# Optimization experiments

Measured on AMD Instinct MI355X. Metric: run time of the kernel, lower is better.

## Reference

```python
import jax, jax.numpy as jnp
import numpy as np

DIM = 128
NUM_LAYERS = 2
FF_MULT = 4
RADIUS = 0.2
K = 8
B, N, L = 8, 2048, 4096
NEG = -1e30


def setup_inputs() -> dict:
    key = jax.random.key(0)
    ks = jax.random.split(key, 12)
    C = DIM
    s = 1.0 / np.sqrt(C)
    w = lambda k, shape, sc: jax.random.normal(k, shape, dtype=jnp.float32) * sc
    inp = {
        "q_xyz": jax.random.uniform(ks[0], (B, N, 3), dtype=jnp.float32),
        "q_feat": jax.random.normal(ks[1], (B, N, C), dtype=jnp.float32),
        "kv_xyz": jax.random.uniform(ks[2], (B, L, 3), dtype=jnp.float32),
        "kv_feat": jax.random.normal(ks[3], (B, L, C), dtype=jnp.float32),
        "kv_pad": jnp.zeros((B, L), dtype=bool),
        # PointTransformerConv params (stacked over layers)
        "W_lin": w(ks[4], (NUM_LAYERS, C, C), s),   # value projection (with bias)
        "b_lin": jnp.zeros((NUM_LAYERS, C), jnp.float32),
        "W_src": w(ks[5], (NUM_LAYERS, C, C), s),   # lin_src, no bias
        "W_dst": w(ks[6], (NUM_LAYERS, C, C), s),   # lin_dst, no bias
        "W_attn": w(ks[7], (NUM_LAYERS, C, C), s),  # attn_nn = Linear+ReLU
        "b_attn": jnp.zeros((NUM_LAYERS, C), jnp.float32),
        "ln1_g": jnp.ones((NUM_LAYERS, C), jnp.float32),
        "ln1_b": jnp.zeros((NUM_LAYERS, C), jnp.float32),
        "W_ff1": w(ks[8], (NUM_LAYERS, C, FF_MULT * C), s),
        "b_ff1": jnp.zeros((NUM_LAYERS, FF_MULT * C), jnp.float32),
        "W_ff2": w(ks[9], (NUM_LAYERS, FF_MULT * C, C), 1.0 / np.sqrt(FF_MULT * C)),
        "b_ff2": jnp.zeros((NUM_LAYERS, C), jnp.float32),
        "ln2_g": jnp.ones((NUM_LAYERS, C), jnp.float32),
        "ln2_b": jnp.zeros((NUM_LAYERS, C), jnp.float32),
    }
    return inp


def _layernorm(x, g, b):
    mu = x.mean(-1, keepdims=True)
    var = ((x - mu) ** 2).mean(-1, keepdims=True)
    return (x - mu) * jax.lax.rsqrt(var + 1e-5) * g + b


def _gather(feats, idx):
    # feats: [B, L, C], idx: [B, N, K] -> [B, N, K, C]
    b, n, k = idx.shape
    g = jnp.take_along_axis(feats, idx.reshape(b, n * k)[:, :, None], axis=1)
    return g.reshape(b, n, k, feats.shape[-1])


def _forward(q_xyz, q_feat, kv_xyz, kv_feat, kv_pad,
             W_lin, b_lin, W_src, W_dst, W_attn, b_attn,
             ln1_g, ln1_b, W_ff1, b_ff1, W_ff2, b_ff2, ln2_g, ln2_b):
    # radius neighbor search (per-batch, fixed K neighbors with validity mask)
    d2 = jnp.sum((q_xyz[:, :, None, :] - kv_xyz[:, None, :, :]) ** 2, axis=-1)  # [B,N,L]
    valid_pair = (d2 <= RADIUS * RADIUS) & (~kv_pad)[:, None, :]
    negd = jnp.where(valid_pair, -d2, NEG)
    negv, idx = jax.lax.top_k(negd, K)          # [B,N,K] nearest-in-ball
    evalid = negv > 0.5 * NEG                   # edge validity mask [B,N,K]

    out = q_feat
    for i in range(NUM_LAYERS):
        # PointTransformerConv, pos_nn = ZeroPos => delta = 0
        aj = _gather(kv_feat @ W_src[i], idx)                    # [B,N,K,C]
        vj = _gather(kv_feat @ W_lin[i] + b_lin[i], idx)         # [B,N,K,C]
        ai = out @ W_dst[i]                                      # [B,N,C]
        logits = jax.nn.relu((ai[:, :, None, :] - aj) @ W_attn[i] + b_attn[i])
        logits = jnp.where(evalid[..., None], logits, NEG)
        m = logits.max(axis=2, keepdims=True)
        e = jnp.exp(logits - m) * evalid[..., None]
        attn = e / jnp.maximum(e.sum(axis=2, keepdims=True), 1e-9)  # per-channel softmax over neighbors
        upd = jnp.sum(attn * vj, axis=2)                         # [B,N,C] scatter-add over edges
        out = _layernorm(out + upd, ln1_g[i], ln1_b[i])
        h = jax.nn.gelu(out @ W_ff1[i] + b_ff1[i], approximate=False)
        out = _layernorm(out + h @ W_ff2[i] + b_ff2[i], ln2_g[i], ln2_b[i])
    return out


def reference(q_xyz, q_feat, kv_xyz, kv_feat, kv_pad,
              W_lin, b_lin, W_src, W_dst, W_attn, b_attn,
              ln1_g, ln1_b, W_ff1, b_ff1, W_ff2, b_ff2, ln2_g, ln2_b):
    return _forward(q_xyz, q_feat, kv_xyz, kv_feat, kv_pad,
                    W_lin, b_lin, W_src, W_dst, W_attn, b_attn,
                    ln1_g, ln1_b, W_ff1, b_ff1, W_ff2, b_ff2, ln2_g, ln2_b)
```

## Files before the change

### kernel.cpp

```cpp
#include <hip/hip_runtime.h>
#include <hip/hip_bf16.h>
#include <math.h>

#define DIM 128
#define BB 8
#define NN 2048
#define LL 4096
#define KK 8

typedef __hip_bfloat16 bf16;
typedef unsigned long long ull;
typedef __attribute__((ext_vector_type(8))) short short8;
typedef __attribute__((ext_vector_type(4))) float float4v;

__device__ __forceinline__ float toF(float x){ return x; }
__device__ __forceinline__ float toF(bf16 x){ return __bfloat162float(x); }
__device__ __forceinline__ void st(float* p, float v){ *p = v; }
__device__ __forceinline__ void st(bf16*  p, float v){ *p = __float2bfloat16(v); }
__device__ __forceinline__ unsigned short f2bf(float f){
  union { bf16 b; unsigned short u; } cv; cv.b = __float2bfloat16(f); return cv.u;
}

__device__ __forceinline__ float gelu_exact(float x){
  return 0.5f * x * (1.0f + erff(x * 0.70710678118654752f));
}

__device__ __forceinline__ float waveSum64(float v){
  #pragma unroll
  for (int o = 32; o > 0; o >>= 1) v += __shfl_xor(v, o, 64);
  return v;
}
__device__ __forceinline__ float quadSum16(float v){
  #pragma unroll
  for (int o = 8; o > 0; o >>= 1) v += __shfl_xor(v, o, 64);
  return v;
}

__device__ __forceinline__ void topk_insert_u(ull (&m)[KK], ull key){
  m[KK-1] = key;
  #pragma unroll
  for (int t = KK-1; t > 0; --t){
    if (m[t] < m[t-1]){ ull tmp = m[t]; m[t] = m[t-1]; m[t-1] = tmp; }
  }
}

#define NCELL 5
#define NC3 125
__global__ __launch_bounds__(1024) void knn_bin(const float* __restrict__ kv_xyz,
                                                float4* __restrict__ bpts,
                                                int* __restrict__ offs )
{
  __shared__ int cnt[NC3];
  __shared__ int off[NC3+1];
  const int b = blockIdx.x;
  const int tid = threadIdx.x;
  if (tid < NC3) cnt[tid] = 0;
  __syncthreads();
  const float* kvp = kv_xyz + (size_t)b * LL * 3;
  float px[4], py[4], pz[4]; int pc[4];
  #pragma unroll
  for (int i = 0; i < 4; i++){
    const int e = tid + i*1024;
    px[i] = kvp[3*e]; py[i] = kvp[3*e+1]; pz[i] = kvp[3*e+2];
    const int cx = min((int)(px[i]*5.f), 4);
    const int cy = min((int)(py[i]*5.f), 4);
    const int cz = min((int)(pz[i]*5.f), 4);
    pc[i] = (cz*5 + cy)*5 + cx;
    atomicAdd(&cnt[pc[i]], 1);
  }
  __syncthreads();
  if (tid == 0){
    int acc = 0;
    for (int c = 0; c < NC3; c++){ off[c] = acc; acc += cnt[c]; }
    off[NC3] = acc;
  }
  __syncthreads();
  if (tid < NC3) cnt[tid] = 0;
  __syncthreads();
  float4* dst = bpts + (size_t)b * LL;
  #pragma unroll
  for (int i = 0; i < 4; i++){
    const int e = tid + i*1024;
    const int pos = off[pc[i]] + atomicAdd(&cnt[pc[i]], 1);
    dst[pos] = make_float4(px[i], py[i], pz[i], __int_as_float(e));
  }
  if (tid < NC3 + 1) offs[b*126 + tid] = off[tid];
}

#define QBLK 8
#define SPL 32
__global__ __launch_bounds__(256) void knn_query(const float* __restrict__ q_xyz,
                                                 const float4* __restrict__ bpts,
                                                 const int* __restrict__ offs,
                                                 int* __restrict__ idx)
{
  __shared__ ull cd[QBLK*257];
  const int tid  = threadIdx.x;
  const int s    = tid >> 3;
  const int qloc = tid & 7;
  const int b    = blockIdx.y;
  const int qbase = blockIdx.x * QBLK;
  const size_t qo = ((size_t)b * NN + qbase + qloc) * 3;
  const float qx = q_xyz[qo], qy = q_xyz[qo+1], qz = q_xyz[qo+2];
  const ull THRKEY = ((ull)0x3D23D70Bu << 32);
  ull kthr = THRKEY;
  ull m[KK];
  #pragma unroll
  for (int k = 0; k < KK; k++) m[k] = ~0ULL;
  const int qcx = min((int)(qx*5.f), 4);
  const int qcy = min((int)(qy*5.f), 4);
  const int qcz = min((int)(qz*5.f), 4);
  const int* ofb = offs + b*126;
  const float4* bp = bpts + (size_t)b * LL;
  const int cx0 = max(qcx-1, 0), cx1 = min(qcx+1, 4);
  for (int cz = max(qcz-1,0); cz <= min(qcz+1,4); cz++){
    for (int cy = max(qcy-1,0); cy <= min(qcy+1,4); cy++){
      const int rowc = (cz*5 + cy)*5;
      const int pstart = ofb[rowc + cx0];
      const int pend   = ofb[rowc + cx1 + 1];
      for (int p = pstart + s; p < pend; p += SPL){
        const float4 pt = bp[p];
        const float dx = qx - pt.x, dy = qy - pt.y, dz = qz - pt.z;
        const float d2 = dx*dx + dy*dy + dz*dz;
        const ull key = ((ull)__float_as_uint(d2) << 32) | (unsigned)__float_as_int(pt.w);
        if (key < kthr){
          topk_insert_u(m, key);
          kthr = (m[KK-1] < THRKEY) ? m[KK-1] : THRKEY;
        }
      }
    }
  }
  #pragma unroll
  for (int k = 0; k < KK; k++) cd[qloc*257 + s*8 + k] = m[k];
  __syncthreads();
  if (tid < 64){
    const int q = tid >> 3, g = tid & 7;
    ull mm[KK];
    #pragma unroll
    for (int k = 0; k < KK; k++) mm[k] = ~0ULL;
    #pragma unroll
    for (int u = 0; u < 4; u++){
      const int sl = g + 8*u;
      #pragma unroll
      for (int k = 0; k < KK; k++){
        const ull key = cd[q*257 + sl*8 + k];
        if (key < mm[KK-1]) topk_insert_u(mm, key);
      }
    }
    #pragma unroll
    for (int k = 0; k < KK; k++) cd[q*257 + g*8 + k] = mm[k];
    if (tid < QBLK){
      ull f[KK];
      #pragma unroll
      for (int k = 0; k < KK; k++) f[k] = ~0ULL;
      for (int j = 0; j < 64; j++){
        const ull key = cd[tid*257 + j];
        if (key < f[KK-1]) topk_insert_u(f, key);
      }
      const int q = b * NN + qbase + tid;
      #pragma unroll
      for (int k = 0; k < KK; k++) idx[q*KK + k] = (int)(unsigned)(f[k] & 0xFFFFFFFFu);
    }
  }
}

__device__ __forceinline__ void packOne(const float* __restrict__ src,
                                        bf16* __restrict__ dst, int idx, int nshift){
  const int k = idx >> nshift;
  const int n = idx & ((1 << nshift) - 1);
  const int N = 1 << nshift;
  st(&dst[((size_t)(k>>3)*N + n)*8 + (k&7)], src[idx]);
}

__global__ __launch_bounds__(256) void prep_weights(const float* __restrict__ Wlin,
                                                    const float* __restrict__ Wff1,
                                                    const float* __restrict__ Wff2,
                                                    const float* __restrict__ Wsrc,
                                                    const float* __restrict__ Wdst,
                                                    const float* __restrict__ Wattn,
                                                    bf16* __restrict__ WlinP,
                                                    bf16* __restrict__ Wff1P,
                                                    bf16* __restrict__ Wff2P,
                                                    bf16* __restrict__ WsaP,
                                                    bf16* __restrict__ WdaP)
{
  __shared__ float row[2][DIM];
  const int bid = blockIdx.x;
  if (bid < 1152){
    int i = bid*256 + threadIdx.x;
    if (i < 32768){
      const int l = i >> 14, r = i & 16383;
      packOne(Wlin + (size_t)l*16384, WlinP + (size_t)l*16384, r, 7);
    } else if (i < 163840){
      i -= 32768;
      const int l = i >> 16, r = i & 65535;
      packOne(Wff1 + (size_t)l*65536, Wff1P + (size_t)l*65536, r, 9);
    } else if (i < 294912){
      i -= 163840;
      const int l = i >> 16, r = i & 65535;
      packOne(Wff2 + (size_t)l*65536, Wff2P + (size_t)l*65536, r, 7);
    }
  } else {
    const int half = threadIdx.x >> 7;
    const int c = threadIdx.x & 127;
    const int tt = (bid - 1152)*2 + half;
    const int r = tt & 127, which = (tt >> 7) & 1, lay = tt >> 8;
    const float* Wx = (which ? Wdst : Wsrc) + (size_t)lay*DIM*DIM;
    const float* Wa = Wattn + (size_t)lay*DIM*DIM;
    row[half][c] = Wx[r*DIM + c];
    __syncthreads();
    float acc = 0.f;
    for (int j = 0; j < DIM; j++) acc = fmaf(row[half][j], Wa[j*DIM + c], acc);
    bf16* dst = (which ? WdaP : WsaP) + (size_t)lay*DIM*DIM;
    st(&dst[((size_t)(r>>3)*DIM + c)*8 + (r&7)], acc);
  }
}

__device__ __forceinline__ void stage_A_f32(const float* __restrict__ A, size_t r0,
                                            int kd, int kc, unsigned short* As, int tid){
  #pragma unroll
  for (int i = 0; i < 8; i++){
    const int f = tid + i*256;
    const int row = f >> 5, c4 = (f & 31) * 4;
    const float4 v = *(const float4*)&A[(r0+row)*kd + kc + c4];
    uint2 u;
    u.x = (unsigned)f2bf(v.x) | ((unsigned)f2bf(v.y) << 16);
    u.y = (unsigned)f2bf(v.z) | ((unsigned)f2bf(v.w) << 16);
    *(uint2*)&As[row*136 + c4] = u;
  }
}
__device__ __forceinline__ void stage_A_bf16(const bf16* __restrict__ A, size_t r0,
                                             int kd, int kc, unsigned short* As, int tid){
  #pragma unroll
  for (int i = 0; i < 8; i++){
    const int f = tid + i*256;
    const int row = f >> 5, c4 = (f & 31) * 4;
    *(uint2*)&As[row*136 + c4] = *(const uint2*)&A[(r0+row)*kd + kc + c4];
  }
}

template<typename TA, int NDIM, bool GELU>
__global__ __launch_bounds__(256) void mfma_single(const TA* __restrict__ A,
                                                   const bf16* __restrict__ Wp,
                                                   const float* __restrict__ bias,
                                                   bf16* __restrict__ Y)
{
  __shared__ __align__(16) unsigned short As[64*136];
  const int tid = threadIdx.x;
  const size_t r0 = (size_t)blockIdx.x * 64;
  const int nblk = blockIdx.y * 128;
  if (sizeof(TA) == 4) stage_A_f32((const float*)A, r0, 128, 0, As, tid);
  else                 stage_A_bf16((const bf16*)A, r0, 128, 0, As, tid);
  __syncthreads();
  const int wid = tid >> 6, ln = tid & 63, qd = ln >> 4, cl = ln & 15;
  float4v acc[8];
  #pragma unroll
  for (int t = 0; t < 8; t++) acc[t] = (float4v){0.f,0.f,0.f,0.f};
  #pragma unroll
  for (int ks = 0; ks < 4; ks++){
    const short8 a = *(const short8*)&As[(wid*16 + cl)*136 + (ks*4 + qd)*8];
    const short8* wb = (const short8*)Wp + (size_t)(ks*4 + qd)*NDIM + nblk + cl;
    #pragma unroll
    for (int t = 0; t < 8; t++){
      const short8 b = wb[t*16];
      acc[t] = __builtin_amdgcn_mfma_f32_16x16x32_bf16(a, b, acc[t], 0, 0, 0);
    }
  }
  #pragma unroll
  for (int t = 0; t < 8; t++){
    const int col = nblk + t*16 + cl;
    const float bv = bias ? bias[col] : 0.f;
    #pragma unroll
    for (int r = 0; r < 4; r++){
      const size_t row = r0 + wid*16 + qd*4 + r;
      float v = acc[t][r] + bv;
      if (GELU) v = gelu_exact(v);
      st(&Y[row*NDIM + col], v);
    }
  }
}

__global__ __launch_bounds__(256) void mfma_dual_qa(const float* __restrict__ kvf,
                                                    const float* __restrict__ featIn,
                                                    const bf16* __restrict__ Wp0,
                                                    const bf16* __restrict__ Wp1,
                                                    const bf16* __restrict__ WpQ,
                                                    const float* __restrict__ bias1,
                                                    bf16* __restrict__ Y0,
                                                    bf16* __restrict__ Y1,
                                                    bf16* __restrict__ Yq)
{
  __shared__ __align__(16) unsigned short As[64*136];
  const int tid = threadIdx.x;
  const int wid = tid >> 6, ln = tid & 63, qd = ln >> 4, cl = ln & 15;
  if (blockIdx.x < 512){
    const size_t r0 = (size_t)blockIdx.x * 64;
    stage_A_f32(kvf, r0, 128, 0, As, tid);
    __syncthreads();
    float4v ac0[8], ac1[8];
    #pragma unroll
    for (int t = 0; t < 8; t++){ ac0[t] = (float4v){0.f,0.f,0.f,0.f}; ac1[t] = (float4v){0.f,0.f,0.f,0.f}; }
    #pragma unroll
    for (int ks = 0; ks < 4; ks++){
      const short8 a = *(const short8*)&As[(wid*16 + cl)*136 + (ks*4 + qd)*8];
      const size_t wo = (size_t)(ks*4 + qd)*DIM + cl;
      const short8* wb0 = (const short8*)Wp0 + wo;
      const short8* wb1 = (const short8*)Wp1 + wo;
      #pragma unroll
      for (int t = 0; t < 8; t++){
        const short8 b0 = wb0[t*16];
        ac0[t] = __builtin_amdgcn_mfma_f32_16x16x32_bf16(a, b0, ac0[t], 0, 0, 0);
        const short8 b1 = wb1[t*16];
        ac1[t] = __builtin_amdgcn_mfma_f32_16x16x32_bf16(a, b1, ac1[t], 0, 0, 0);
      }
    }
    #pragma unroll
    for (int t = 0; t < 8; t++){
      const int col = t*16 + cl;
      const float bv = bias1[col];
      #pragma unroll
      for (int r = 0; r < 4; r++){
        const size_t row = r0 + wid*16 + qd*4 + r;
        st(&Y0[row*DIM + col], ac0[t][r]);
        st(&Y1[row*DIM + col], ac1[t][r] + bv);
      }
    }
  } else {
    const size_t r0 = (size_t)(blockIdx.x - 512) * 64;
    stage_A_f32(featIn, r0, 128, 0, As, tid);
    __syncthreads();
    float4v acc[8];
    #pragma unroll
    for (int t = 0; t < 8; t++) acc[t] = (float4v){0.f,0.f,0.f,0.f};
    #pragma unroll
    for (int ks = 0; ks < 4; ks++){
      const short8 a = *(const short8*)&As[(wid*16 + cl)*136 + (ks*4 + qd)*8];
      const short8* wb = (const short8*)WpQ + (size_t)(ks*4 + qd)*DIM + cl;
      #pragma unroll
      for (int t = 0; t < 8; t++){
        const short8 b = wb[t*16];
        acc[t] = __builtin_amdgcn_mfma_f32_16x16x32_bf16(a, b, acc[t], 0, 0, 0);
      }
    }
    #pragma unroll
    for (int t = 0; t < 8; t++){
      const int col = t*16 + cl;
      #pragma unroll
      for (int r = 0; r < 4; r++){
        const size_t row = r0 + wid*16 + qd*4 + r;
        st(&Yq[row*DIM + col], acc[t][r]);
      }
    }
  }
}

__global__ __launch_bounds__(256) void mfma_ff2ln(const bf16* __restrict__ A,
                                                  const bf16* __restrict__ Wp,
                                                  const float* __restrict__ b2,
                                                  const bf16* __restrict__ resid,
                                                  const float* __restrict__ g,
                                                  const float* __restrict__ bb,
                                                  float* __restrict__ Y)
{
  __shared__ __align__(16) unsigned short As[64*136];
  const int tid = threadIdx.x;
  const size_t r0 = (size_t)blockIdx.x * 64;
  const int wid = tid >> 6, ln = tid & 63, qd = ln >> 4, cl = ln & 15;
  float4v acc[8];
  #pragma unroll
  for (int t = 0; t < 8; t++) acc[t] = (float4v){0.f,0.f,0.f,0.f};
  for (int kc = 0; kc < 512; kc += 128){
    __syncthreads();
    stage_A_bf16(A, r0, 512, kc, As, tid);
    __syncthreads();
    const int k8c = kc >> 3;
    #pragma unroll
    for (int ks = 0; ks < 4; ks++){
      const short8 a = *(const short8*)&As[(wid*16 + cl)*136 + (ks*4 + qd)*8];
      const short8* wb = (const short8*)Wp + (size_t)(k8c + ks*4 + qd)*DIM + cl;
      #pragma unroll
      for (int t = 0; t < 8; t++){
        const short8 b = wb[t*16];
        acc[t] = __builtin_amdgcn_mfma_f32_16x16x32_bf16(a, b, acc[t], 0, 0, 0);
      }
    }
  }
  float v[8][4];
  #pragma unroll
  for (int t = 0; t < 8; t++){
    const int col = t*16 + cl;
    const float bv = b2[col];
    #pragma unroll
    for (int r = 0; r < 4; r++){
      const size_t row = r0 + wid*16 + qd*4 + r;
      v[t][r] = acc[t][r] + bv + toF(resid[row*DIM + col]);
    }
  }
  #pragma unroll
  for (int r = 0; r < 4; r++){
    float s = 0.f;
    #pragma unroll
    for (int t = 0; t < 8; t++) s += v[t][r];
    const float mu = quadSum16(s) * (1.f/DIM);
    float q = 0.f;
    #pragma unroll
    for (int t = 0; t < 8; t++){ const float d = v[t][r] - mu; q += d*d; }
    const float inv = rsqrtf(quadSum16(q) * (1.f/DIM) + 1e-5f);
    const size_t row = r0 + wid*16 + qd*4 + r;
    #pragma unroll
    for (int t = 0; t < 8; t++){
      const int col = t*16 + cl;
      Y[row*DIM + col] = (v[t][r] - mu) * inv * g[col] + bb[col];
    }
  }
}

__global__ __launch_bounds__(256) void attn_ln1(const bf16* __restrict__ qA,
                                                const bf16* __restrict__ srcA,
                                                const bf16* __restrict__ linp,
                                                const int* __restrict__ idx,
                                                const float* __restrict__ b_attn,
                                                const float* __restrict__ feat,
                                                const float* __restrict__ g,
                                                const float* __restrict__ bb,
                                                bf16* __restrict__ out1)
{
  const int tid = threadIdx.x;
  const int wv = tid >> 6, ln = tid & 63;
  const int q = blockIdx.x * 4 + wv;
  const int b = q >> 11;
  const bf16* sbase = srcA + (size_t)b * LL * DIM;
  const bf16* vbase = linp + (size_t)b * LL * DIM;
  const int c0 = ln, c1 = ln + 64;
  const float qa0 = toF(qA[(size_t)q*DIM + c0]) + b_attn[c0];
  const float qa1 = toF(qA[(size_t)q*DIM + c1]) + b_attn[c1];
  int ids[KK]; float l0[KK], l1[KK];
  float m0 = -1e30f, m1 = -1e30f;
  #pragma unroll
  for (int k = 0; k < KK; k++){
    const int id = idx[q*KK + k]; ids[k] = id;
    if (id >= 0){
      const float s0 = toF(sbase[(size_t)id*DIM + c0]);
      const float s1 = toF(sbase[(size_t)id*DIM + c1]);
      l0[k] = fmaxf(qa0 - s0, 0.f); m0 = fmaxf(m0, l0[k]);
      l1[k] = fmaxf(qa1 - s1, 0.f); m1 = fmaxf(m1, l1[k]);
    } else { l0[k] = 0.f; l1[k] = 0.f; }
  }
  float sum0 = 0.f, sum1 = 0.f, upd0 = 0.f, upd1 = 0.f;
  #pragma unroll
  for (int k = 0; k < KK; k++) if (ids[k] >= 0){
    const float e0 = expf(l0[k] - m0); l0[k] = e0; sum0 += e0;
    const float e1 = expf(l1[k] - m1); l1[k] = e1; sum1 += e1;
  }
  if (sum0 > 0.f){
    const float i0 = 1.f / sum0, i1 = 1.f / sum1;
    #pragma unroll
    for (int k = 0; k < KK; k++) if (ids[k] >= 0){
      upd0 = fmaf(l0[k]*i0, toF(vbase[(size_t)ids[k]*DIM + c0]), upd0);
      upd1 = fmaf(l1[k]*i1, toF(vbase[(size_t)ids[k]*DIM + c1]), upd1);
    }
  }
  const float x0 = feat[(size_t)q*DIM + c0] + upd0;
  const float x1 = feat[(size_t)q*DIM + c1] + upd1;
  const float mu = waveSum64(x0 + x1) * (1.f/DIM);
  const float d0 = x0 - mu, d1 = x1 - mu;
  const float var = waveSum64(d0*d0 + d1*d1) * (1.f/DIM);
  const float inv = rsqrtf(var + 1e-5f);
  st(&out1[(size_t)q*DIM + c0], d0 * inv * g[c0] + bb[c0]);
  st(&out1[(size_t)q*DIM + c1], d1 * inv * g[c1] + bb[c1]);
}

extern "C" void kernel_launch(void* const* d_in, const int* in_sizes, int n_in,
                              void* d_out, int out_size, void* d_ws, size_t ws_size,
                              hipStream_t stream)
{
  const float* q_xyz  = (const float*)d_in[0];
  const float* q_feat = (const float*)d_in[1];
  const float* kv_xyz = (const float*)d_in[2];
  const float* kv_feat= (const float*)d_in[3];
  const float* W_lin  = (const float*)d_in[5];
  const float* b_lin  = (const float*)d_in[6];
  const float* W_src  = (const float*)d_in[7];
  const float* W_dst  = (const float*)d_in[8];
  const float* W_attn = (const float*)d_in[9];
  const float* b_attn = (const float*)d_in[10];
  const float* ln1_g  = (const float*)d_in[11];
  const float* ln1_b  = (const float*)d_in[12];
  const float* W_ff1  = (const float*)d_in[13];
  const float* b_ff1  = (const float*)d_in[14];
  const float* W_ff2  = (const float*)d_in[15];
  const float* b_ff2  = (const float*)d_in[16];
  const float* ln2_g  = (const float*)d_in[17];
  const float* ln2_b  = (const float*)d_in[18];
  float* out = (float*)d_out;

  const int MQ  = BB * NN;
  const int MKV = BB * LL;

  char* p = (char*)d_ws;
  int*    idxb  = (int*)p;    p += (size_t)MQ * KK * 4;
  float4* bpts  = (float4*)p; p += (size_t)BB * LL * 16;
  int*    boffs = (int*)p;    p += (size_t)BB * 126 * 4;
  bf16*  WsaP  = (bf16*)p;  p += (size_t)2 * DIM * DIM * 2;
  bf16*  WdaP  = (bf16*)p;  p += (size_t)2 * DIM * DIM * 2;
  bf16*  WlinP = (bf16*)p;  p += (size_t)2 * DIM * DIM * 2;
  bf16*  Wff1P = (bf16*)p;  p += (size_t)2 * DIM * 4*DIM * 2;
  bf16*  Wff2P = (bf16*)p;  p += (size_t)2 * 4*DIM * DIM * 2;
  float* feat  = (float*)p; p += (size_t)MQ * DIM * 4;
  bf16*  out1  = (bf16*)p;  p += (size_t)MQ * DIM * 2;
  bf16*  srcA  = (bf16*)p;  p += (size_t)MKV * DIM * 2;
  bf16*  linp  = (bf16*)p;  p += (size_t)MKV * DIM * 2;
  bf16*  qA    = (bf16*)p;  p += (size_t)MQ * DIM * 2;
  bf16*  hbuf  = srcA;

  knn_bin<<<BB, 1024, 0, stream>>>(kv_xyz, bpts, boffs);
  knn_query<<<dim3(NN/QBLK, BB), 256, 0, stream>>>(q_xyz, bpts, boffs, idxb);
  prep_weights<<<1152 + 256, 256, 0, stream>>>(W_lin, W_ff1, W_ff2, W_src, W_dst,
                                               W_attn, WlinP, Wff1P, Wff2P, WsaP, WdaP);

  for (int i = 0; i < 2; i++){
    const size_t w128 = (size_t)i * DIM * DIM;
    const size_t w512 = (size_t)i * DIM * 4*DIM;
    const float* featIn = (i == 0) ? q_feat : feat;

    mfma_dual_qa<<<MKV/64 + MQ/64, 256, 0, stream>>>(kv_feat, featIn,
        WsaP + w128, WlinP + w128, WdaP + w128, b_lin + i*DIM, srcA, linp, qA);
    attn_ln1<<<MQ/4, 256, 0, stream>>>(qA, srcA, linp, idxb, b_attn + i*DIM, featIn,
                                       ln1_g + i*DIM, ln1_b + i*DIM, out1);
    mfma_single<bf16, 512, true><<<dim3(MQ/64, 4), 256, 0, stream>>>(
        out1, Wff1P + w512, b_ff1 + i*4*DIM, hbuf);
    float* ydst = (i == 1) ? out : feat;
    mfma_ff2ln<<<MQ/64, 256, 0, stream>>>(hbuf, Wff2P + w512, b_ff2 + i*DIM, out1,
                                          ln2_g + i*DIM, ln2_b + i*DIM, ydst);
  }
}
```

Before: 302.6 us.

## Fuse attention, LN1, FFN and LN2 into one kernel; sort queries by grid cell

Attention aggregation, the first layernorm, the FF1+GELU GEMM and the FF2+layernorm GEMM now run in one per-wave kernel. Each wave keeps its 16 rows and the 512-wide hidden activations in LDS, so the out1 and hidden buffers no longer make global-memory round trips and two launches per layer go away. Separately, query points are binned by spatial cell so each knn_query block works on nearby queries, which should make neighbour scans more uniform within a block and cache-friendlier. The trade-off is much more LDS per block (about 87 KB), which lowers occupancy, and 16 serial attention rows per wave before the MFMA work starts.

```diff
diff --git a/kernel.cpp b/kernel.cpp
--- a/kernel.cpp
+++ b/kernel.cpp
@@ -15,6 +15,9 @@
 
 __device__ __forceinline__ float toF(float x){ return x; }
 __device__ __forceinline__ float toF(bf16 x){ return __bfloat162float(x); }
+__device__ __forceinline__ float bfuToF(unsigned short u){
+  return __uint_as_float((unsigned)u << 16);
+}
 __device__ __forceinline__ void st(float* p, float v){ *p = v; }
 __device__ __forceinline__ void st(bf16*  p, float v){ *p = __float2bfloat16(v); }
 __device__ __forceinline__ unsigned short f2bf(float f){
@@ -44,47 +47,80 @@
   }
 }
 
-#define NCELL 5
 #define NC3 125
 __global__ __launch_bounds__(1024) void knn_bin(const float* __restrict__ kv_xyz,
+                                                const float* __restrict__ q_xyz,
                                                 float4* __restrict__ bpts,
-                                                int* __restrict__ offs )
+                                                int* __restrict__ offs ,
+                                                int* __restrict__ qsrt )
 {
   __shared__ int cnt[NC3];
   __shared__ int off[NC3+1];
-  const int b = blockIdx.x;
+  const int b   = blockIdx.x & 7;
+  const int role= blockIdx.x >> 3;
   const int tid = threadIdx.x;
   if (tid < NC3) cnt[tid] = 0;
   __syncthreads();
-  const float* kvp = kv_xyz + (size_t)b * LL * 3;
-  float px[4], py[4], pz[4]; int pc[4];
-  #pragma unroll
-  for (int i = 0; i < 4; i++){
-    const int e = tid + i*1024;
-    px[i] = kvp[3*e]; py[i] = kvp[3*e+1]; pz[i] = kvp[3*e+2];
-    const int cx = min((int)(px[i]*5.f), 4);
-    const int cy = min((int)(py[i]*5.f), 4);
-    const int cz = min((int)(pz[i]*5.f), 4);
-    pc[i] = (cz*5 + cy)*5 + cx;
-    atomicAdd(&cnt[pc[i]], 1);
-  }
-  __syncthreads();
-  if (tid == 0){
-    int acc = 0;
-    for (int c = 0; c < NC3; c++){ off[c] = acc; acc += cnt[c]; }
-    off[NC3] = acc;
-  }
-  __syncthreads();
-  if (tid < NC3) cnt[tid] = 0;
-  __syncthreads();
-  float4* dst = bpts + (size_t)b * LL;
-  #pragma unroll
-  for (int i = 0; i < 4; i++){
-    const int e = tid + i*1024;
-    const int pos = off[pc[i]] + atomicAdd(&cnt[pc[i]], 1);
-    dst[pos] = make_float4(px[i], py[i], pz[i], __int_as_float(e));
-  }
-  if (tid < NC3 + 1) offs[b*126 + tid] = off[tid];
+  if (role == 0){
+    const float* kvp = kv_xyz + (size_t)b * LL * 3;
+    float px[4], py[4], pz[4]; int pc[4];
+    #pragma unroll
+    for (int i = 0; i < 4; i++){
+      const int e = tid + i*1024;
+      px[i] = kvp[3*e]; py[i] = kvp[3*e+1]; pz[i] = kvp[3*e+2];
+      const int cx = min((int)(px[i]*5.f), 4);
+      const int cy = min((int)(py[i]*5.f), 4);
+      const int cz = min((int)(pz[i]*5.f), 4);
+      pc[i] = (cz*5 + cy)*5 + cx;
+      atomicAdd(&cnt[pc[i]], 1);
+    }
+    __syncthreads();
+    if (tid == 0){
+      int acc = 0;
+      for (int c = 0; c < NC3; c++){ off[c] = acc; acc += cnt[c]; }
+      off[NC3] = acc;
+    }
+    __syncthreads();
+    if (tid < NC3) cnt[tid] = 0;
+    __syncthreads();
+    float4* dst = bpts + (size_t)b * LL;
+    #pragma unroll
+    for (int i = 0; i < 4; i++){
+      const int e = tid + i*1024;
+      const int pos = off[pc[i]] + atomicAdd(&cnt[pc[i]], 1);
+      dst[pos] = make_float4(px[i], py[i], pz[i], __int_as_float(e));
+    }
+    if (tid < NC3 + 1) offs[b*126 + tid] = off[tid];
+  } else {
+    const float* qp = q_xyz + (size_t)b * NN * 3;
+    int pc[2];
+    #pragma unroll
+    for (int i = 0; i < 2; i++){
+      const int e = tid + i*1024;
+      const float x = qp[3*e], y = qp[3*e+1], z = qp[3*e+2];
+      const int cx = min((int)(x*5.f), 4);
+      const int cy = min((int)(y*5.f), 4);
+      const int cz = min((int)(z*5.f), 4);
+      pc[i] = (cz*5 + cy)*5 + cx;
+      atomicAdd(&cnt[pc[i]], 1);
+    }
+    __syncthreads();
+    if (tid == 0){
+      int acc = 0;
+      for (int c = 0; c < NC3; c++){ off[c] = acc; acc += cnt[c]; }
+      off[NC3] = acc;
+    }
+    __syncthreads();
+    if (tid < NC3) cnt[tid] = 0;
+    __syncthreads();
+    int* dst = qsrt + (size_t)b * NN;
+    #pragma unroll
+    for (int i = 0; i < 2; i++){
+      const int e = tid + i*1024;
+      const int pos = off[pc[i]] + atomicAdd(&cnt[pc[i]], 1);
+      dst[pos] = e;
+    }
+  }
 }
 
 #define QBLK 8
@@ -92,6 +128,7 @@
 __global__ __launch_bounds__(256) void knn_query(const float* __restrict__ q_xyz,
                                                  const float4* __restrict__ bpts,
                                                  const int* __restrict__ offs,
+                                                 const int* __restrict__ qsrt,
                                                  int* __restrict__ idx)
 {
   __shared__ ull cd[QBLK*257];
@@ -100,7 +137,8 @@
   const int qloc = tid & 7;
   const int b    = blockIdx.y;
   const int qbase = blockIdx.x * QBLK;
-  const size_t qo = ((size_t)b * NN + qbase + qloc) * 3;
+  const int qid = qsrt[b*NN + qbase + qloc];
+  const size_t qo = ((size_t)b * NN + qid) * 3;
   const float qx = q_xyz[qo], qy = q_xyz[qo+1], qz = q_xyz[qo+2];
   const ull THRKEY = ((ull)0x3D23D70Bu << 32);
   ull kthr = THRKEY;
@@ -157,9 +195,9 @@
         const ull key = cd[tid*257 + j];
         if (key < f[KK-1]) topk_insert_u(f, key);
       }
-      const int q = b * NN + qbase + tid;
-      #pragma unroll
-      for (int k = 0; k < KK; k++) idx[q*KK + k] = (int)(unsigned)(f[k] & 0xFFFFFFFFu);
+      const int oq = b * NN + qsrt[b*NN + qbase + tid];
+      #pragma unroll
+      for (int k = 0; k < KK; k++) idx[oq*KK + k] = (int)(unsigned)(f[k] & 0xFFFFFFFFu);
     }
   }
 }
@@ -229,56 +267,6 @@
     *(uint2*)&As[row*136 + c4] = u;
   }
 }
-__device__ __forceinline__ void stage_A_bf16(const bf16* __restrict__ A, size_t r0,
-                                             int kd, int kc, unsigned short* As, int tid){
-  #pragma unroll
-  for (int i = 0; i < 8; i++){
-    const int f = tid + i*256;
-    const int row = f >> 5, c4 = (f & 31) * 4;
-    *(uint2*)&As[row*136 + c4] = *(const uint2*)&A[(r0+row)*kd + kc + c4];
-  }
-}
-
-template<typename TA, int NDIM, bool GELU>
-__global__ __launch_bounds__(256) void mfma_single(const TA* __restrict__ A,
-                                                   const bf16* __restrict__ Wp,
-                                                   const float* __restrict__ bias,
-                                                   bf16* __restrict__ Y)
-{
-  __shared__ __align__(16) unsigned short As[64*136];
-  const int tid = threadIdx.x;
-  const size_t r0 = (size_t)blockIdx.x * 64;
-  const int nblk = blockIdx.y * 128;
-  if (sizeof(TA) == 4) stage_A_f32((const float*)A, r0, 128, 0, As, tid);
-  else                 stage_A_bf16((const bf16*)A, r0, 128, 0, As, tid);
-  __syncthreads();
-  const int wid = tid >> 6, ln = tid & 63, qd = ln >> 4, cl = ln & 15;
-  float4v acc[8];
-  #pragma unroll
-  for (int t = 0; t < 8; t++) acc[t] = (float4v){0.f,0.f,0.f,0.f};
-  #pragma unroll
-  for (int ks = 0; ks < 4; ks++){
-    const short8 a = *(const short8*)&As[(wid*16 + cl)*136 + (ks*4 + qd)*8];
-    const short8* wb = (const short8*)Wp + (size_t)(ks*4 + qd)*NDIM + nblk + cl;
-    #pragma unroll
-    for (int t = 0; t < 8; t++){
-      const short8 b = wb[t*16];
-      acc[t] = __builtin_amdgcn_mfma_f32_16x16x32_bf16(a, b, acc[t], 0, 0, 0);
-    }
-  }
-  #pragma unroll
-  for (int t = 0; t < 8; t++){
-    const int col = nblk + t*16 + cl;
-    const float bv = bias ? bias[col] : 0.f;
-    #pragma unroll
-    for (int r = 0; r < 4; r++){
-      const size_t row = r0 + wid*16 + qd*4 + r;
-      float v = acc[t][r] + bv;
-      if (GELU) v = gelu_exact(v);
-      st(&Y[row*NDIM + col], v);
-    }
-  }
-}
 
 __global__ __launch_bounds__(256) void mfma_dual_qa(const float* __restrict__ kvf,
                                                     const float* __restrict__ featIn,
@@ -354,34 +342,108 @@
   }
 }
 
-__global__ __launch_bounds__(256) void mfma_ff2ln(const bf16* __restrict__ A,
-                                                  const bf16* __restrict__ Wp,
-                                                  const float* __restrict__ b2,
-                                                  const bf16* __restrict__ resid,
-                                                  const float* __restrict__ g,
-                                                  const float* __restrict__ bb,
-                                                  float* __restrict__ Y)
+__global__ __launch_bounds__(256) void attn_ff(const bf16* __restrict__ qA,
+                                               const bf16* __restrict__ srcA,
+                                               const bf16* __restrict__ linp,
+                                               const int* __restrict__ idx,
+                                               const float* __restrict__ b_attn,
+                                               const float* __restrict__ featIn,
+                                               const float* __restrict__ g1,
+                                               const float* __restrict__ bb1,
+                                               const bf16* __restrict__ W1p,
+                                               const float* __restrict__ b1,
+                                               const bf16* __restrict__ W2p,
+                                               const float* __restrict__ b2,
+                                               const float* __restrict__ g2,
+                                               const float* __restrict__ bb2,
+                                               float* __restrict__ Y)
 {
-  __shared__ __align__(16) unsigned short As[64*136];
+  __shared__ __align__(16) unsigned short As[4][16*136];
+  __shared__ __align__(16) unsigned short Hs[4][4][16*136];
   const int tid = threadIdx.x;
-  const size_t r0 = (size_t)blockIdx.x * 64;
-  const int wid = tid >> 6, ln = tid & 63, qd = ln >> 4, cl = ln & 15;
-  float4v acc[8];
-  #pragma unroll
-  for (int t = 0; t < 8; t++) acc[t] = (float4v){0.f,0.f,0.f,0.f};
-  for (int kc = 0; kc < 512; kc += 128){
-    __syncthreads();
-    stage_A_bf16(A, r0, 512, kc, As, tid);
-    __syncthreads();
-    const int k8c = kc >> 3;
+  const int w = tid >> 6, ln = tid & 63, qd = ln >> 4, cl = ln & 15;
+  const int q0 = blockIdx.x * 64 + w * 16;
+  for (int j = 0; j < 16; j++){
+    const int q = q0 + j;
+    const int b = q >> 11;
+    const bf16* sbase = srcA + (size_t)b * LL * DIM;
+    const bf16* vbase = linp + (size_t)b * LL * DIM;
+    const int c0 = ln, c1 = ln + 64;
+    const float qa0 = toF(qA[(size_t)q*DIM + c0]) + b_attn[c0];
+    const float qa1 = toF(qA[(size_t)q*DIM + c1]) + b_attn[c1];
+    int ids[KK]; float l0[KK], l1[KK];
+    float m0 = -1e30f, m1 = -1e30f;
+    #pragma unroll
+    for (int k = 0; k < KK; k++){
+      const int id = idx[q*KK + k]; ids[k] = id;
+      if (id >= 0){
+        l0[k] = fmaxf(qa0 - toF(sbase[(size_t)id*DIM + c0]), 0.f); m0 = fmaxf(m0, l0[k]);
+        l1[k] = fmaxf(qa1 - toF(sbase[(size_t)id*DIM + c1]), 0.f); m1 = fmaxf(m1, l1[k]);
+      } else { l0[k] = 0.f; l1[k] = 0.f; }
+    }
+    float sum0 = 0.f, sum1 = 0.f, upd0 = 0.f, upd1 = 0.f;
+    #pragma unroll
+    for (int k = 0; k < KK; k++) if (ids[k] >= 0){
+      const float e0 = expf(l0[k] - m0); l0[k] = e0; sum0 += e0;
+      const float e1 = expf(l1[k] - m1); l1[k] = e1; sum1 += e1;
+    }
+    if (sum0 > 0.f){
+      const float i0 = 1.f / sum0, i1 = 1.f / sum1;
+      #pragma unroll
+      for (int k = 0; k < KK; k++) if (ids[k] >= 0){
+        upd0 = fmaf(l0[k]*i0, toF(vbase[(size_t)ids[k]*DIM + c0]), upd0);
+        upd1 = fmaf(l1[k]*i1, toF(vbase[(size_t)ids[k]*DIM + c1]), upd1);
+      }
+    }
+    const float x0 = featIn[(size_t)q*DIM + c0] + upd0;
+    const float x1 = featIn[(size_t)q*DIM + c1] + upd1;
+    const float mu = waveSum64(x0 + x1) * (1.f/DIM);
+    const float d0 = x0 - mu, d1 = x1 - mu;
+    const float var = waveSum64(d0*d0 + d1*d1) * (1.f/DIM);
+    const float inv = rsqrtf(var + 1e-5f);
+    As[w][j*136 + c0] = f2bf(d0 * inv * g1[c0] + bb1[c0]);
+    As[w][j*136 + c1] = f2bf(d1 * inv * g1[c1] + bb1[c1]);
+  }
+  #pragma unroll
+  for (int half = 0; half < 2; half++){
+    float4v acc[16];
+    #pragma unroll
+    for (int t = 0; t < 16; t++) acc[t] = (float4v){0.f,0.f,0.f,0.f};
     #pragma unroll
     for (int ks = 0; ks < 4; ks++){
-      const short8 a = *(const short8*)&As[(wid*16 + cl)*136 + (ks*4 + qd)*8];
-      const short8* wb = (const short8*)Wp + (size_t)(k8c + ks*4 + qd)*DIM + cl;
+      const short8 a = *(const short8*)&As[w][cl*136 + (ks*4 + qd)*8];
+      const short8* wb = (const short8*)W1p + (size_t)(ks*4 + qd)*512 + half*256 + cl;
+      #pragma unroll
+      for (int t = 0; t < 16; t++){
+        const short8 b = wb[t*16];
+        acc[t] = __builtin_amdgcn_mfma_f32_16x16x32_bf16(a, b, acc[t], 0, 0, 0);
+      }
+    }
+    #pragma unroll
+    for (int t = 0; t < 16; t++){
+      const int col = half*256 + t*16 + cl;
+      const float bv = b1[col];
+      const int chunk = half*2 + (t >> 3);
+      #pragma unroll
+      for (int r = 0; r < 4; r++){
+        Hs[w][chunk][(qd*4 + r)*136 + (t & 7)*16 + cl] = f2bf(gelu_exact(acc[t][r] + bv));
+      }
+    }
+  }
+  float4v a2[8];
+  #pragma unroll
+  for (int t = 0; t < 8; t++) a2[t] = (float4v){0.f,0.f,0.f,0.f};
+  #pragma unroll
+  for (int chunk = 0; chunk < 4; chunk++){
+    #pragma unroll
+    for (int ks = 0; ks < 4; ks++){
+      const short8 a = *(const short8*)&Hs[w][chunk][cl*136 + (ks*4 + qd)*8];
+      const int k8 = chunk*16 + ks*4 + qd;
+      const short8* wb = (const short8*)W2p + (size_t)k8*DIM + cl;
       #pragma unroll
       for (int t = 0; t < 8; t++){
         const short8 b = wb[t*16];
-        acc[t] = __builtin_amdgcn_mfma_f32_16x16x32_bf16(a, b, acc[t], 0, 0, 0);
+        a2[t] = __builtin_amdgcn_mfma_f32_16x16x32_bf16(a, b, a2[t], 0, 0, 0);
       }
     }
   }
@@ -392,8 +454,7 @@
     const float bv = b2[col];
     #pragma unroll
     for (int r = 0; r < 4; r++){
-      const size_t row = r0 + wid*16 + qd*4 + r;
-      v[t][r] = acc[t][r] + bv + toF(resid[row*DIM + col]);
+      v[t][r] = a2[t][r] + bv + bfuToF(As[w][(qd*4 + r)*136 + col]);
     }
   }
   #pragma unroll
@@ -402,72 +463,17 @@
     #pragma unroll
     for (int t = 0; t < 8; t++) s += v[t][r];
     const float mu = quadSum16(s) * (1.f/DIM);
-    float q = 0.f;
-    #pragma unroll
-    for (int t = 0; t < 8; t++){ const float d = v[t][r] - mu; q += d*d; }
-    const float inv = rsqrtf(quadSum16(q) * (1.f/DIM) + 1e-5f);
-    const size_t row = r0 + wid*16 + qd*4 + r;
+    float qv = 0.f;
+    #pragma unroll
+    for (int t = 0; t < 8; t++){ const float d = v[t][r] - mu; qv += d*d; }
+    const float inv = rsqrtf(quadSum16(qv) * (1.f/DIM) + 1e-5f);
+    const size_t row = q0 + qd*4 + r;
     #pragma unroll
     for (int t = 0; t < 8; t++){
       const int col = t*16 + cl;
-      Y[row*DIM + col] = (v[t][r] - mu) * inv * g[col] + bb[col];
-    }
-  }
-}
-
-__global__ __launch_bounds__(256) void attn_ln1(const bf16* __restrict__ qA,
-                                                const bf16* __restrict__ srcA,
-                                                const bf16* __restrict__ linp,
-                                                const int* __restrict__ idx,
-                                                const float* __restrict__ b_attn,
-                                                const float* __restrict__ feat,
-                                                const float* __restrict__ g,
-                                                const float* __restrict__ bb,
-                                                bf16* __restrict__ out1)
-{
-  const int tid = threadIdx.x;
-  const int wv = tid >> 6, ln = tid & 63;
-  const int q = blockIdx.x * 4 + wv;
-  const int b = q >> 11;
-  const bf16* sbase = srcA + (size_t)b * LL * DIM;
-  const bf16* vbase = linp + (size_t)b * LL * DIM;
-  const int c0 = ln, c1 = ln + 64;
-  const float qa0 = toF(qA[(size_t)q*DIM + c0]) + b_attn[c0];
-  const float qa1 = toF(qA[(size_t)q*DIM + c1]) + b_attn[c1];
-  int ids[KK]; float l0[KK], l1[KK];
-  float m0 = -1e30f, m1 = -1e30f;
-  #pragma unroll
-  for (int k = 0; k < KK; k++){
-    const int id = idx[q*KK + k]; ids[k] = id;
-    if (id >= 0){
-      const float s0 = toF(sbase[(size_t)id*DIM + c0]);
-      const float s1 = toF(sbase[(size_t)id*DIM + c1]);
-      l0[k] = fmaxf(qa0 - s0, 0.f); m0 = fmaxf(m0, l0[k]);
-      l1[k] = fmaxf(qa1 - s1, 0.f); m1 = fmaxf(m1, l1[k]);
-    } else { l0[k] = 0.f; l1[k] = 0.f; }
-  }
-  float sum0 = 0.f, sum1 = 0.f, upd0 = 0.f, upd1 = 0.f;
-  #pragma unroll
-  for (int k = 0; k < KK; k++) if (ids[k] >= 0){
-    const float e0 = expf(l0[k] - m0); l0[k] = e0; sum0 += e0;
-    const float e1 = expf(l1[k] - m1); l1[k] = e1; sum1 += e1;
-  }
-  if (sum0 > 0.f){
-    const float i0 = 1.f / sum0, i1 = 1.f / sum1;
-    #pragma unroll
-    for (int k = 0; k < KK; k++) if (ids[k] >= 0){
-      upd0 = fmaf(l0[k]*i0, toF(vbase[(size_t)ids[k]*DIM + c0]), upd0);
-      upd1 = fmaf(l1[k]*i1, toF(vbase[(size_t)ids[k]*DIM + c1]), upd1);
-    }
-  }
-  const float x0 = feat[(size_t)q*DIM + c0] + upd0;
-  const float x1 = feat[(size_t)q*DIM + c1] + upd1;
-  const float mu = waveSum64(x0 + x1) * (1.f/DIM);
-  const float d0 = x0 - mu, d1 = x1 - mu;
-  const float var = waveSum64(d0*d0 + d1*d1) * (1.f/DIM);
-  const float inv = rsqrtf(var + 1e-5f);
-  st(&out1[(size_t)q*DIM + c0], d0 * inv * g[c0] + bb[c0]);
-  st(&out1[(size_t)q*DIM + c1], d1 * inv * g[c1] + bb[c1]);
+      Y[row*DIM + col] = (v[t][r] - mu) * inv * g2[col] + bb2[col];
+    }
+  }
 }
 
 extern "C" void kernel_launch(void* const* d_in, const int* in_sizes, int n_in,
@@ -501,20 +507,19 @@
   int*    idxb  = (int*)p;    p += (size_t)MQ * KK * 4;
   float4* bpts  = (float4*)p; p += (size_t)BB * LL * 16;
   int*    boffs = (int*)p;    p += (size_t)BB * 126 * 4;
+  int*    qsrt  = (int*)p;    p += (size_t)BB * NN * 4;
   bf16*  WsaP  = (bf16*)p;  p += (size_t)2 * DIM * DIM * 2;
   bf16*  WdaP  = (bf16*)p;  p += (size_t)2 * DIM * DIM * 2;
   bf16*  WlinP = (bf16*)p;  p += (size_t)2 * DIM * DIM * 2;
   bf16*  Wff1P = (bf16*)p;  p += (size_t)2 * DIM * 4*DIM * 2;
   bf16*  Wff2P = (bf16*)p;  p += (size_t)2 * 4*DIM * DIM * 2;
   float* feat  = (float*)p; p += (size_t)MQ * DIM * 4;
-  bf16*  out1  = (bf16*)p;  p += (size_t)MQ * DIM * 2;
   bf16*  srcA  = (bf16*)p;  p += (size_t)MKV * DIM * 2;
   bf16*  linp  = (bf16*)p;  p += (size_t)MKV * DIM * 2;
   bf16*  qA    = (bf16*)p;  p += (size_t)MQ * DIM * 2;
-  bf16*  hbuf  = srcA;
-
-  knn_bin<<<BB, 1024, 0, stream>>>(kv_xyz, bpts, boffs);
-  knn_query<<<dim3(NN/QBLK, BB), 256, 0, stream>>>(q_xyz, bpts, boffs, idxb);
+
+  knn_bin<<<16, 1024, 0, stream>>>(kv_xyz, q_xyz, bpts, boffs, qsrt);
+  knn_query<<<dim3(NN/QBLK, BB), 256, 0, stream>>>(q_xyz, bpts, boffs, qsrt, idxb);
   prep_weights<<<1152 + 256, 256, 0, stream>>>(W_lin, W_ff1, W_ff2, W_src, W_dst,
                                                W_attn, WlinP, Wff1P, Wff2P, WsaP, WdaP);
 
@@ -525,12 +530,11 @@
 
     mfma_dual_qa<<<MKV/64 + MQ/64, 256, 0, stream>>>(kv_feat, featIn,
         WsaP + w128, WlinP + w128, WdaP + w128, b_lin + i*DIM, srcA, linp, qA);
-    attn_ln1<<<MQ/4, 256, 0, stream>>>(qA, srcA, linp, idxb, b_attn + i*DIM, featIn,
-                                       ln1_g + i*DIM, ln1_b + i*DIM, out1);
-    mfma_single<bf16, 512, true><<<dim3(MQ/64, 4), 256, 0, stream>>>(
-        out1, Wff1P + w512, b_ff1 + i*4*DIM, hbuf);
     float* ydst = (i == 1) ? out : feat;
-    mfma_ff2ln<<<MQ/64, 256, 0, stream>>>(hbuf, Wff2P + w512, b_ff2 + i*DIM, out1,
-                                          ln2_g + i*DIM, ln2_b + i*DIM, ydst);
-  }
-}
+    attn_ff<<<MQ/64, 256, 0, stream>>>(qA, srcA, linp, idxb, b_attn + i*DIM, featIn,
+                                       ln1_g + i*DIM, ln1_b + i*DIM,
+                                       Wff1P + w512, b_ff1 + i*4*DIM,
+                                       Wff2P + w512, b_ff2 + i*DIM,
+                                       ln2_g + i*DIM, ln2_b + i*DIM, ydst);
+  }
+}
```

Result: slower. 467.1 us (+54.3%).

## Process queries in spatially sorted cell order for KNN and attention

Applied to the files above, without the earlier changes.

Adds a counting sort of query points into the 5x5x5 spatial grid, run by extra blocks in the binning kernel, and stores the resulting permutation. The KNN query kernel and the attention kernel then visit queries in that sorted order while still writing results to the original query positions. Nearby queries in a block then scan the same cells and gather overlapping neighbour rows, which is meant to cut divergence in the neighbour search and improve cache reuse in the attention gathers. The cost is an extra indirection load per query and scattered output writes.

```diff
diff --git a/kernel.cpp b/kernel.cpp
--- a/kernel.cpp
+++ b/kernel.cpp
@@ -44,47 +44,80 @@
   }
 }
 
-#define NCELL 5
 #define NC3 125
 __global__ __launch_bounds__(1024) void knn_bin(const float* __restrict__ kv_xyz,
+                                                const float* __restrict__ q_xyz,
                                                 float4* __restrict__ bpts,
-                                                int* __restrict__ offs )
+                                                int* __restrict__ offs ,
+                                                int* __restrict__ qsrt )
 {
   __shared__ int cnt[NC3];
   __shared__ int off[NC3+1];
-  const int b = blockIdx.x;
+  const int b   = blockIdx.x & 7;
+  const int role= blockIdx.x >> 3;
   const int tid = threadIdx.x;
   if (tid < NC3) cnt[tid] = 0;
   __syncthreads();
-  const float* kvp = kv_xyz + (size_t)b * LL * 3;
-  float px[4], py[4], pz[4]; int pc[4];
-  #pragma unroll
-  for (int i = 0; i < 4; i++){
-    const int e = tid + i*1024;
-    px[i] = kvp[3*e]; py[i] = kvp[3*e+1]; pz[i] = kvp[3*e+2];
-    const int cx = min((int)(px[i]*5.f), 4);
-    const int cy = min((int)(py[i]*5.f), 4);
-    const int cz = min((int)(pz[i]*5.f), 4);
-    pc[i] = (cz*5 + cy)*5 + cx;
-    atomicAdd(&cnt[pc[i]], 1);
-  }
-  __syncthreads();
-  if (tid == 0){
-    int acc = 0;
-    for (int c = 0; c < NC3; c++){ off[c] = acc; acc += cnt[c]; }
-    off[NC3] = acc;
-  }
-  __syncthreads();
-  if (tid < NC3) cnt[tid] = 0;
-  __syncthreads();
-  float4* dst = bpts + (size_t)b * LL;
-  #pragma unroll
-  for (int i = 0; i < 4; i++){
-    const int e = tid + i*1024;
-    const int pos = off[pc[i]] + atomicAdd(&cnt[pc[i]], 1);
-    dst[pos] = make_float4(px[i], py[i], pz[i], __int_as_float(e));
-  }
-  if (tid < NC3 + 1) offs[b*126 + tid] = off[tid];
+  if (role == 0){
+    const float* kvp = kv_xyz + (size_t)b * LL * 3;
+    float px[4], py[4], pz[4]; int pc[4];
+    #pragma unroll
+    for (int i = 0; i < 4; i++){
+      const int e = tid + i*1024;
+      px[i] = kvp[3*e]; py[i] = kvp[3*e+1]; pz[i] = kvp[3*e+2];
+      const int cx = min((int)(px[i]*5.f), 4);
+      const int cy = min((int)(py[i]*5.f), 4);
+      const int cz = min((int)(pz[i]*5.f), 4);
+      pc[i] = (cz*5 + cy)*5 + cx;
+      atomicAdd(&cnt[pc[i]], 1);
+    }
+    __syncthreads();
+    if (tid == 0){
+      int acc = 0;
+      for (int c = 0; c < NC3; c++){ off[c] = acc; acc += cnt[c]; }
+      off[NC3] = acc;
+    }
+    __syncthreads();
+    if (tid < NC3) cnt[tid] = 0;
+    __syncthreads();
+    float4* dst = bpts + (size_t)b * LL;
+    #pragma unroll
+    for (int i = 0; i < 4; i++){
+      const int e = tid + i*1024;
+      const int pos = off[pc[i]] + atomicAdd(&cnt[pc[i]], 1);
+      dst[pos] = make_float4(px[i], py[i], pz[i], __int_as_float(e));
+    }
+    if (tid < NC3 + 1) offs[b*126 + tid] = off[tid];
+  } else {
+    const float* qp = q_xyz + (size_t)b * NN * 3;
+    int pc[2];
+    #pragma unroll
+    for (int i = 0; i < 2; i++){
+      const int e = tid + i*1024;
+      const float x = qp[3*e], y = qp[3*e+1], z = qp[3*e+2];
+      const int cx = min((int)(x*5.f), 4);
+      const int cy = min((int)(y*5.f), 4);
+      const int cz = min((int)(z*5.f), 4);
+      pc[i] = (cz*5 + cy)*5 + cx;
+      atomicAdd(&cnt[pc[i]], 1);
+    }
+    __syncthreads();
+    if (tid == 0){
+      int acc = 0;
+      for (int c = 0; c < NC3; c++){ off[c] = acc; acc += cnt[c]; }
+      off[NC3] = acc;
+    }
+    __syncthreads();
+    if (tid < NC3) cnt[tid] = 0;
+    __syncthreads();
+    int* dst = qsrt + (size_t)b * NN;
+    #pragma unroll
+    for (int i = 0; i < 2; i++){
+      const int e = tid + i*1024;
+      const int pos = off[pc[i]] + atomicAdd(&cnt[pc[i]], 1);
+      dst[pos] = e;
+    }
+  }
 }
 
 #define QBLK 8
@@ -92,6 +125,7 @@
 __global__ __launch_bounds__(256) void knn_query(const float* __restrict__ q_xyz,
                                                  const float4* __restrict__ bpts,
                                                  const int* __restrict__ offs,
+                                                 const int* __restrict__ qsrt,
                                                  int* __restrict__ idx)
 {
   __shared__ ull cd[QBLK*257];
@@ -100,7 +134,8 @@
   const int qloc = tid & 7;
   const int b    = blockIdx.y;
   const int qbase = blockIdx.x * QBLK;
-  const size_t qo = ((size_t)b * NN + qbase + qloc) * 3;
+  const int qid = qsrt[b*NN + qbase + qloc];
+  const size_t qo = ((size_t)b * NN + qid) * 3;
   const float qx = q_xyz[qo], qy = q_xyz[qo+1], qz = q_xyz[qo+2];
   const ull THRKEY = ((ull)0x3D23D70Bu << 32);
   ull kthr = THRKEY;
@@ -157,9 +192,9 @@
         const ull key = cd[tid*257 + j];
         if (key < f[KK-1]) topk_insert_u(f, key);
       }
-      const int q = b * NN + qbase + tid;
-      #pragma unroll
-      for (int k = 0; k < KK; k++) idx[q*KK + k] = (int)(unsigned)(f[k] & 0xFFFFFFFFu);
+      const int oq = b * NN + qsrt[b*NN + qbase + tid];
+      #pragma unroll
+      for (int k = 0; k < KK; k++) idx[oq*KK + k] = (int)(unsigned)(f[k] & 0xFFFFFFFFu);
     }
   }
 }
@@ -419,6 +454,7 @@
                                                 const bf16* __restrict__ srcA,
                                                 const bf16* __restrict__ linp,
                                                 const int* __restrict__ idx,
+                                                const int* __restrict__ qsrt,
                                                 const float* __restrict__ b_attn,
                                                 const float* __restrict__ feat,
                                                 const float* __restrict__ g,
@@ -427,8 +463,9 @@
 {
   const int tid = threadIdx.x;
   const int wv = tid >> 6, ln = tid & 63;
-  const int q = blockIdx.x * 4 + wv;
-  const int b = q >> 11;
+  const int sp = blockIdx.x * 4 + wv;
+  const int b = sp >> 11;
+  const int q = b * NN + qsrt[b*NN + (sp & 2047)];
   const bf16* sbase = srcA + (size_t)b * LL * DIM;
   const bf16* vbase = linp + (size_t)b * LL * DIM;
   const int c0 = ln, c1 = ln + 64;
@@ -501,6 +538,7 @@
   int*    idxb  = (int*)p;    p += (size_t)MQ * KK * 4;
   float4* bpts  = (float4*)p; p += (size_t)BB * LL * 16;
   int*    boffs = (int*)p;    p += (size_t)BB * 126 * 4;
+  int*    qsrt  = (int*)p;    p += (size_t)BB * NN * 4;
   bf16*  WsaP  = (bf16*)p;  p += (size_t)2 * DIM * DIM * 2;
   bf16*  WdaP  = (bf16*)p;  p += (size_t)2 * DIM * DIM * 2;
   bf16*  WlinP = (bf16*)p;  p += (size_t)2 * DIM * DIM * 2;
@@ -513,8 +551,8 @@
   bf16*  qA    = (bf16*)p;  p += (size_t)MQ * DIM * 2;
   bf16*  hbuf  = srcA;
 
-  knn_bin<<<BB, 1024, 0, stream>>>(kv_xyz, bpts, boffs);
-  knn_query<<<dim3(NN/QBLK, BB), 256, 0, stream>>>(q_xyz, bpts, boffs, idxb);
+  knn_bin<<<16, 1024, 0, stream>>>(kv_xyz, q_xyz, bpts, boffs, qsrt);
+  knn_query<<<dim3(NN/QBLK, BB), 256, 0, stream>>>(q_xyz, bpts, boffs, qsrt, idxb);
   prep_weights<<<1152 + 256, 256, 0, stream>>>(W_lin, W_ff1, W_ff2, W_src, W_dst,
                                                W_attn, WlinP, Wff1P, Wff2P, WsaP, WdaP);
 
@@ -525,8 +563,8 @@
 
     mfma_dual_qa<<<MKV/64 + MQ/64, 256, 0, stream>>>(kv_feat, featIn,
         WsaP + w128, WlinP + w128, WdaP + w128, b_lin + i*DIM, srcA, linp, qA);
-    attn_ln1<<<MQ/4, 256, 0, stream>>>(qA, srcA, linp, idxb, b_attn + i*DIM, featIn,
-                                       ln1_g + i*DIM, ln1_b + i*DIM, out1);
+    attn_ln1<<<MQ/4, 256, 0, stream>>>(qA, srcA, linp, idxb, qsrt, b_attn + i*DIM,
+                                       featIn, ln1_g + i*DIM, ln1_b + i*DIM, out1);
     mfma_single<bf16, 512, true><<<dim3(MQ/64, 4), 256, 0, stream>>>(
         out1, Wff1P + w512, b_ff1 + i*4*DIM, hbuf);
     float* ydst = (i == 1) ? out : feat;
```

Result: no change. 297.4 us (-1.7%).
